# Optimization experiments

Hardware: AMD Instinct MI355X
Metric: run time of the kernel (lower is better)

## Reference

```python
import jax, jax.numpy as jnp
import numpy as np

D_MODEL = 512; FPQ = 15; SEQ = 2048; BSZ = 2
D_STATE = 16; D_CONV = 4; HEADDIM = 64; NHEADS = 16
D_INNER = 1024; CONV_DIM = D_INNER + 2 * D_STATE
D_IN_PROJ = 2 * D_INNER + 2 * D_STATE + NHEADS  # 2096
D_FF = 2048  # mlp_ratio 4.0 * 512
EPS_GATE = 0.01


def _rmsnorm(x, w, eps):
    xf = x.astype(jnp.float32)
    v = jnp.mean(xf * xf, axis=-1, keepdims=True)
    return w * (xf * jax.lax.rsqrt(v + eps)).astype(x.dtype)


def _mamba2(x, inproj, convw, convb, dtbias, Alog, Dp, normw, outproj):
    b, l, _ = x.shape
    zxbcdt = x @ inproj.T                      # [b,l,2096]
    z = zxbcdt[..., :D_INNER]
    xBC = zxbcdt[..., D_INNER:D_INNER + CONV_DIM]
    dt = zxbcdt[..., D_INNER + CONV_DIM:]      # [b,l,h]
    # causal depthwise conv1d (kernel D_CONV) + SiLU
    xp = jnp.pad(xBC, ((0, 0), (D_CONV - 1, 0), (0, 0)))
    conv = convb + sum(xp[:, k:k + l, :] * convw[:, k] for k in range(D_CONV))
    xBC = jax.nn.silu(conv)
    xs = xBC[..., :D_INNER]
    Bm = xBC[..., D_INNER:D_INNER + D_STATE]   # [b,l,n]
    Cm = xBC[..., D_INNER + D_STATE:]          # [b,l,n]
    dt = jax.nn.softplus(dt + dtbias)          # [b,l,h]
    A = -jnp.exp(Alog)                         # [h]
    xh = xs.reshape(b, l, NHEADS, HEADDIM)     # [b,l,h,p]
    dA = jnp.exp(dt * A)                       # [b,l,h]

    def step(hst, inp):
        dA_t, dt_t, B_t, x_t, C_t = inp        # [b,h],[b,h],[b,n],[b,h,p],[b,n]
        hst = dA_t[:, :, None, None] * hst + jnp.einsum('bh,bn,bhp->bhpn', dt_t, B_t, x_t)
        return hst, jnp.einsum('bhpn,bn->bhp', hst, C_t)

    h0 = jnp.zeros((b, NHEADS, HEADDIM, D_STATE), x.dtype)
    _, ys = jax.lax.scan(step, h0, (dA.transpose(1, 0, 2), dt.transpose(1, 0, 2),
                                    Bm.transpose(1, 0, 2), xh.transpose(1, 0, 2, 3),
                                    Cm.transpose(1, 0, 2)))
    y = ys.transpose(1, 0, 2, 3) + Dp[None, None, :, None] * xh  # [b,l,h,p]
    y = y.reshape(b, l, D_INNER) * jax.nn.silu(z)                # gated
    y = _rmsnorm(y, normw, 1e-5)
    return y @ outproj.T


def _forward(hidden_states, norm1_w, wfc_w, wfc_b, gfc_w, gfc_b,
             f_inproj, f_convw, f_convb, f_dtbias, f_Alog, f_D, f_normw, f_outproj,
             b_inproj, b_convw, b_convb, b_dtbias, b_Alog, b_D, b_normw, b_outproj,
             norm2_w, fc1_w, fc1_b, fc2_w, fc2_b):
    residual = hidden_states
    h = _rmsnorm(hidden_states, norm1_w, 1e-6)
    bsz, seq_len, d = h.shape
    cq = FPQ + 1
    nck = seq_len // cq
    h4 = h.reshape(bsz, nck, cq, d)
    frames = h4[:, :, :FPQ, :]                       # [b,nc,FPQ,d]
    queries = h4[:, :, FPQ, :]                       # [b,nc,d]
    alpha = jax.nn.softmax(queries @ wfc_w.T + wfc_b, axis=-1)   # [b,nc,FPQ]
    agg = jnp.einsum('bcfd,bcf->bcd', frames, alpha)
    gate = jax.nn.sigmoid(queries @ gfc_w.T + gfc_b)             # [b,nc,1]
    gate = gate * (1 - 2 * EPS_GATE) + EPS_GATE
    qn = queries * (1 - gate) + agg * gate
    h4 = jnp.concatenate([frames, qn[:, :, None, :]], axis=2)
    h = h4.reshape(bsz, seq_len, d)
    out_fwd = _mamba2(h, f_inproj, f_convw, f_convb, f_dtbias, f_Alog, f_D, f_normw, f_outproj)
    out_bwd = jnp.flip(_mamba2(jnp.flip(h, 1), b_inproj, b_convw, b_convb, b_dtbias, b_Alog, b_D, b_normw, b_outproj), 1)
    h = out_fwd + out_bwd + residual
    rm = h
    h = _rmsnorm(h, norm2_w, 1e-6)
    h = jax.nn.silu(h @ fc1_w.T + fc1_b) @ fc2_w.T + fc2_b
    h = h + rm
    return h + residual


def setup_inputs() -> dict:
    key = jax.random.key(0)
    ks = jax.random.split(key, 16)

    def n(k, shape, s=0.02):
        return s * jax.random.normal(k, shape, jnp.float32)

    def mixer(kb):
        k = jax.random.split(kb, 6)
        dtv = jnp.exp(jax.random.uniform(k[3], (NHEADS,), minval=jnp.log(1e-3), maxval=jnp.log(0.1)))
        return dict(
            inproj=n(k[0], (D_IN_PROJ, D_MODEL)),
            convw=n(k[1], (CONV_DIM, D_CONV), 0.2),
            convb=jnp.zeros((CONV_DIM,), jnp.float32),
            dtbias=jnp.log(jnp.expm1(dtv)),
            Alog=jnp.log(jax.random.uniform(k[4], (NHEADS,), minval=1.0, maxval=16.0)),
            D=jnp.ones((NHEADS,), jnp.float32),
            normw=jnp.ones((D_INNER,), jnp.float32),
            outproj=n(k[2], (D_MODEL, D_INNER)),
        )

    mf = mixer(ks[1]); mb = mixer(ks[2])
    inp = {
        'hidden_states': jax.random.normal(ks[0], (BSZ, SEQ, D_MODEL), jnp.float32),
        'norm1_w': jnp.ones((D_MODEL,), jnp.float32),
        'wfc_w': n(ks[3], (FPQ, D_MODEL)) * 0.001,
        'wfc_b': jnp.zeros((FPQ,), jnp.float32),
        'gfc_w': n(ks[4], (1, D_MODEL)) * 0.001,
        'gfc_b': jnp.zeros((1,), jnp.float32),
        'norm2_w': jnp.ones((D_MODEL,), jnp.float32),
        'fc1_w': n(ks[5], (D_FF, D_MODEL)),
        'fc1_b': jnp.zeros((D_FF,), jnp.float32),
        'fc2_w': n(ks[6], (D_MODEL, D_FF)),
        'fc2_b': jnp.zeros((D_MODEL,), jnp.float32),
    }
    for pre, m in (('f_', mf), ('b_', mb)):
        for kname, v in m.items():
            inp[pre + kname] = v
    return inp


def reference(hidden_states, norm1_w, wfc_w, wfc_b, gfc_w, gfc_b,
              f_inproj, f_convw, f_convb, f_dtbias, f_Alog, f_D, f_normw, f_outproj,
              b_inproj, b_convw, b_convb, b_dtbias, b_Alog, b_D, b_normw, b_outproj,
              norm2_w, fc1_w, fc1_b, fc2_w, fc2_b):
    return _forward(hidden_states, norm1_w, wfc_w, wfc_b, gfc_w, gfc_b,
                    f_inproj, f_convw, f_convb, f_dtbias, f_Alog, f_D, f_normw, f_outproj,
                    b_inproj, b_convw, b_convb, b_dtbias, b_Alog, b_D, b_normw, b_outproj,
                    norm2_w, fc1_w, fc1_b, fc2_w, fc2_b)
```

## Files before the change

kernel.cpp:

```cpp
#include <hip/hip_runtime.h>
#include <math.h>

#define SEQ 2048
#define BSZ 2
#define DM 512
#define DIN 1024
#define DSTATE 16
#define NH 16
#define HD 64
#define CONVDIM 1056
#define DINPROJ 2096
#define DFF 2048
#define ROWS (BSZ*SEQ)
#define NCH 32
#define CT  (SEQ/NCH)
#define ZXW 2176
#define ZXBN 8912896ull
#define BCN 65536ull
#define DTN 65536ull
#define YN  4194304ull
#define HSN 1048576ull

typedef short bf16x8 __attribute__((ext_vector_type(8)));
typedef float f32x4  __attribute__((ext_vector_type(4)));
typedef unsigned short u16x8 __attribute__((ext_vector_type(8)));

__device__ __forceinline__ float sigf(float x){ return 1.f/(1.f+expf(-x)); }

__device__ __forceinline__ unsigned short f2bf(float f){
  union { float f; unsigned u; } v; v.f = f;
  unsigned r = (v.u + 0x7FFFu + ((v.u >> 16) & 1u)) >> 16;
  return (unsigned short)r;
}
__device__ __forceinline__ float bf2f(unsigned short h){
  union { unsigned u; float f; } v; v.u = ((unsigned)h) << 16;
  return v.f;
}

template<int N> __device__ __forceinline__ void s_wait_vmcnt(){
  if constexpr (N == 0)      asm volatile("s_waitcnt vmcnt(0)" ::: "memory");
  else if constexpr (N == 1) asm volatile("s_waitcnt vmcnt(1)" ::: "memory");
  else if constexpr (N == 2) asm volatile("s_waitcnt vmcnt(2)" ::: "memory");
  else if constexpr (N == 3) asm volatile("s_waitcnt vmcnt(3)" ::: "memory");
  else if constexpr (N == 4) asm volatile("s_waitcnt vmcnt(4)" ::: "memory");
  else                       asm volatile("s_waitcnt vmcnt(8)" ::: "memory");
}

__device__ __forceinline__ float wave_reduce(float v){
#pragma unroll
  for (int o = 32; o > 0; o >>= 1) v += __shfl_down(v, o);
  return v;
}

__device__ __forceinline__ float block_reduce_256(float v, float* sbuf){
  v = wave_reduce(v);
  int lane = threadIdx.x & 63, wid = threadIdx.x >> 6;
  if (lane == 0) sbuf[wid] = v;
  __syncthreads();
  float s = sbuf[0] + sbuf[1] + sbuf[2] + sbuf[3];
  __syncthreads();
  return s;
}

__global__ __launch_bounds__(256)
void castpad2_k(const float* __restrict__ in0, const float* __restrict__ in1,
                unsigned short* __restrict__ out0, unsigned short* __restrict__ out1,
                int N, int K, int Npad){
  int tot = Npad*K;
  int idx = blockIdx.x*256 + threadIdx.x;
  const float* in = in0; unsigned short* out = out0;
  if (idx >= tot){ idx -= tot; in = in1; out = out1; }
  if (idx >= tot) return;
  int n = idx / K, k = idx - n*K;
  out[idx] = (n < N) ? f2bf(in[(size_t)n*K + k]) : (unsigned short)0;
}

struct Cast6 {
  const float* src[6];
  unsigned short* dst[6];
  int n[6];
};
__global__ __launch_bounds__(256)
void cast6_k(Cast6 cp){
  int seg = blockIdx.y;
  int n4 = cp.n[seg] >> 2;
  int i = blockIdx.x*256 + threadIdx.x;
  if (i >= n4) return;
  const float* src = cp.src[seg];
  unsigned short* dst = cp.dst[seg];
  float4 v = *(const float4*)&src[i*4];
  ushort4 o;
  o.x = f2bf(v.x); o.y = f2bf(v.y); o.z = f2bf(v.z); o.w = f2bf(v.w);
  *(ushort4*)&dst[i*4] = o;
}

__global__ __launch_bounds__(256)
void rmsnorm512_k(const float* __restrict__ x, const float* __restrict__ w,
                  float* __restrict__ y, unsigned short* __restrict__ yb, float eps){
  __shared__ float sbuf[4];
  int r = blockIdx.x;
  const float* xr = x + (size_t)r*DM;
  float v0 = xr[threadIdx.x];
  float v1 = xr[threadIdx.x + 256];
  float ss = block_reduce_256(v0*v0 + v1*v1, sbuf);
  float rs = rsqrtf(ss*(1.f/DM) + eps);
  float o0 = w[threadIdx.x]*v0*rs;
  float o1 = w[threadIdx.x+256]*v1*rs;
  y[(size_t)r*DM + threadIdx.x]       = o0;
  y[(size_t)r*DM + threadIdx.x + 256] = o1;
  yb[(size_t)r*DM + threadIdx.x]       = f2bf(o0);
  yb[(size_t)r*DM + threadIdx.x + 256] = f2bf(o1);
}

__global__ __launch_bounds__(256)
void gated_fusion_k(float* __restrict__ h, unsigned short* __restrict__ hb,
                    const float* __restrict__ wfc_w, const float* __restrict__ wfc_b,
                    const float* __restrict__ gfc_w, const float* __restrict__ gfc_b){
  int c = blockIdx.x;
  float* base = h + (size_t)c*16*DM;
  float* qrow = base + 15*DM;
  unsigned short* qrow_b = hb + (size_t)c*16*DM + 15*DM;
  __shared__ float q[DM];
  __shared__ float dots[16];
  for (int i = threadIdx.x; i < DM; i += 256) q[i] = qrow[i];
  __syncthreads();
  int wid = threadIdx.x >> 6, lane = threadIdx.x & 63;
  for (int f = wid; f < 16; f += 4){
    const float* wf = (f < 15) ? (wfc_w + (size_t)f*DM) : gfc_w;
    float s = 0.f;
    for (int i = lane; i < DM; i += 64) s += q[i]*wf[i];
    s = wave_reduce(s);
    if (lane == 0) dots[f] = s;
  }
  __syncthreads();
  if (threadIdx.x == 0){
    float mx = -1e30f;
    for (int f = 0; f < 15; f++){ dots[f] += wfc_b[f]; mx = fmaxf(mx, dots[f]); }
    float sum = 0.f;
    for (int f = 0; f < 15; f++){ float e = expf(dots[f]-mx); dots[f] = e; sum += e; }
    float inv = 1.f/sum;
    for (int f = 0; f < 15; f++) dots[f] *= inv;
    float g = sigf(dots[15] + gfc_b[0]);
    dots[15] = g*0.98f + 0.01f;
  }
  __syncthreads();
  float gate = dots[15];
  for (int d = threadIdx.x; d < DM; d += 256){
    float agg = 0.f;
#pragma unroll
    for (int f = 0; f < 15; f++) agg += base[(size_t)f*DM + d]*dots[f];
    float qn = q[d]*(1.f-gate) + agg*gate;
    qrow[d] = qn;
    qrow_b[d] = f2bf(qn);
  }
}

template<int NW, int WM, int WN, int FM, int FN, int DEPTH, int NBUF>
__global__ __launch_bounds__(NW*64)
void mgemm_k(const unsigned short* __restrict__ A, size_t Astride,
             const unsigned short* __restrict__ W0, const unsigned short* __restrict__ W1,
             const float* __restrict__ bias, const float* __restrict__ add1,
             const float* __restrict__ add2, float* __restrict__ Cf,
             unsigned short* __restrict__ Cb, size_t Cstride,
             int K, int Nreal, int flipArg, int act){
  constexpr int BM = WM*FM*16;
  constexpr int BN = WN*FN*16;
  constexpr int NG = (BM+BN)/16;
  constexpr int L  = NG/NW;
  static_assert(NG % NW == 0, "staging must be uniform per wave");
  constexpr int BUFS = (BM+BN)*32;
  __shared__ __align__(16) unsigned short S[NBUF*BUFS];
  int tid = threadIdx.x;
  int w = tid >> 6, lane = tid & 63;
  int gx = gridDim.x;
  int nwg = gx*gridDim.y;
  int bid = blockIdx.x + gx*blockIdx.y;
  int swz = (bid & 7)*(nwg >> 3) + (bid >> 3);
  int n0 = (swz % gx)*BN, m0 = (swz / gx)*BM;
  int dir = blockIdx.z;
  const unsigned short* Aa = A + (size_t)dir*Astride;
  const unsigned short* Wd = dir ? W1 : W0;
  int flip = (flipArg < 0) ? dir : flipArg;
  int wr = w / WN, wc = w % WN;

  f32x4 acc[FM][FN];
#pragma unroll
  for (int i = 0; i < FM; i++)
#pragma unroll
    for (int j = 0; j < FN; j++)
#pragma unroll
      for (int r = 0; r < 4; r++) acc[i][j][r] = 0.f;

  const unsigned short* gp[L];
  int gdst[L];
#pragma unroll
  for (int gi = 0; gi < L; gi++){
    int g = w + gi*NW;
    int r16 = lane >> 2, cch = lane & 3;
    int r = g*16 + r16;
    const unsigned short* src;
    if (r < BM){
      int gm = m0 + r;
      if (flip) gm = (gm & ~(SEQ-1)) | ((SEQ-1) - (gm & (SEQ-1)));
      src = Aa + (size_t)gm*K;
    } else {
      src = Wd + (size_t)(n0 + (r - BM))*K;
    }
    int c2 = (cch + ((r16 >> 1) & 3)) & 3;
    gp[gi] = src + c2*8;
    gdst[gi] = g*16*32;
  }
  int aoff[FM], boff[FN];
#pragma unroll
  for (int i = 0; i < FM; i++){
    int R = wr*FM*16 + i*16 + (lane & 15);
    int slot = ((lane >> 4) - ((R >> 1) & 3)) & 3;
    aoff[i] = R*32 + slot*8;
  }
#pragma unroll
  for (int j = 0; j < FN; j++){
    int R = BM + wc*FN*16 + j*16 + (lane & 15);
    int slot = ((lane >> 4) - ((R >> 1) & 3)) & 3;
    boff[j] = R*32 + slot*8;
  }

  int T = K >> 5;
#pragma unroll
  for (int jt = 0; jt < DEPTH; jt++){
#pragma unroll
    for (int gi = 0; gi < L; gi++)
      __builtin_amdgcn_global_load_lds(
        (const __attribute__((address_space(1))) void*)(gp[gi] + (jt << 5)),
        (__attribute__((address_space(3))) void*)&S[jt*BUFS + gdst[gi]], 16, 0, 0);
  }

  int cs = 0;
  for (int t = 0; t < T; t++){
    int rem = T - 1 - t;
    if (rem >= DEPTH-1)             s_wait_vmcnt<L*(DEPTH-1)>();
    else if constexpr (DEPTH >= 3){ if (rem == 1) s_wait_vmcnt<L>(); else s_wait_vmcnt<0>(); }
    else                            s_wait_vmcnt<0>();
    __builtin_amdgcn_s_barrier();
    __builtin_amdgcn_sched_barrier(0);
    const unsigned short* buf = &S[cs*BUFS];
    bf16x8 af[FM], bfr[FN];
#pragma unroll
    for (int i = 0; i < FM; i++) af[i] = *(const bf16x8*)&buf[aoff[i]];
#pragma unroll
    for (int j = 0; j < FN; j++) bfr[j] = *(const bf16x8*)&buf[boff[j]];
    if constexpr (NBUF == DEPTH){
      asm volatile("s_waitcnt lgkmcnt(0)" ::: "memory");
      __builtin_amdgcn_sched_barrier(0);
      __builtin_amdgcn_s_barrier();
    }
    if (t + DEPTH < T){
      int ss = cs + DEPTH; if (ss >= NBUF) ss -= NBUF;
#pragma unroll
      for (int gi = 0; gi < L; gi++)
        __builtin_amdgcn_global_load_lds(
          (const __attribute__((address_space(1))) void*)(gp[gi] + ((t + DEPTH) << 5)),
          (__attribute__((address_space(3))) void*)&S[ss*BUFS + gdst[gi]], 16, 0, 0);
    }
#pragma unroll
    for (int i = 0; i < FM; i++)
#pragma unroll
      for (int j = 0; j < FN; j++)
        acc[i][j] = __builtin_amdgcn_mfma_f32_16x16x32_bf16(af[i], bfr[j], acc[i][j], 0, 0, 0);
    cs = (cs + 1 == NBUF) ? 0 : cs + 1;
  }

  float* Cfd = Cf ? Cf + (size_t)dir*Cstride : nullptr;
  unsigned short* Cbd = Cb ? Cb + (size_t)dir*Cstride : nullptr;

  if (Cbd){
    __syncthreads();
#pragma unroll
    for (int i = 0; i < FM; i++){
#pragma unroll
      for (int j = 0; j < FN; j++){
        int col = wc*FN*16 + j*16 + (lane & 15);
        float bv = bias ? bias[n0 + col] : 0.f;
#pragma unroll
        for (int r = 0; r < 4; r++){
          int row = wr*FM*16 + i*16 + (lane >> 4)*4 + r;
          float x = acc[i][j][r] + bv;
          if (act) x = x*sigf(x);
          S[row*BN + (col ^ ((row & 3) << 3))] = f2bf(x);
        }
      }
    }
    __syncthreads();
    constexpr int TOT8 = BM*BN/8;
    for (int s = tid; s < TOT8; s += NW*64){
      int idx = s*8;
      int row = idx / BN, col = idx % BN;
      u16x8 v = *(const u16x8*)&S[row*BN + (col ^ ((row & 3) << 3))];
      *(u16x8*)&Cbd[(size_t)(m0 + row)*Nreal + n0 + col] = v;
    }
    return;
  }

  int mbase = m0 + wr*FM*16 + (lane >> 4)*4;
  int nbase = n0 + wc*FN*16 + (lane & 15);
#pragma unroll
  for (int i = 0; i < FM; i++){
#pragma unroll
    for (int j = 0; j < FN; j++){
      int col = nbase + j*16;
      if (col < Nreal){
        float bv = bias ? bias[col] : 0.f;
#pragma unroll
        for (int r = 0; r < 4; r++){
          size_t idx = (size_t)(mbase + i*16 + r)*Nreal + col;
          float x = acc[i][j][r] + bv;
          if (act) x = x*sigf(x);
          if (add1) x += add1[idx] + add2[idx];
          Cfd[idx] = x;
        }
      }
    }
  }
}

__global__ __launch_bounds__(128)
void convbc_dt_k(const unsigned short* __restrict__ zxb,
                 const float* __restrict__ convw0, const float* __restrict__ convw1,
                 const float* __restrict__ convb0, const float* __restrict__ convb1,
                 const float* __restrict__ dtbias0, const float* __restrict__ dtbias1,
                 const float* __restrict__ Alog0, const float* __restrict__ Alog1,
                 float* __restrict__ Bm, float* __restrict__ Cm,
                 float* __restrict__ dtv, float* __restrict__ dAv){
  int dir = blockIdx.y;
  const unsigned short* zb = zxb + (size_t)dir*ZXBN;
  int r0 = blockIdx.x*4;
  int l0 = r0 & (SEQ-1);
  int rbase = r0 - l0;
  int tid = threadIdx.x;
  if (tid < 32){
    const float* convw = dir ? convw1 : convw0;
    const float* convb = dir ? convb1 : convb0;
    int cc = 1024 + tid;
    int col = 2048 + tid;
    float w0 = convw[cc*4+0], w1 = convw[cc*4+1], w2 = convw[cc*4+2], w3 = convw[cc*4+3];
    float bv = convb[cc];
    float v[7];
#pragma unroll
    for (int i = 0; i < 7; i++){
      int ls = l0 - 3 + i;
      v[i] = (ls >= 0) ? bf2f(zb[(size_t)(rbase+ls)*ZXW + col]) : 0.f;
    }
#pragma unroll
    for (int j = 0; j < 4; j++){
      float acc = bv + v[j]*w0 + v[j+1]*w1 + v[j+2]*w2 + v[j+3]*w3;
      float val = acc*sigf(acc);
      int r = r0 + j;
      if (tid < 16) Bm[(size_t)dir*BCN + (size_t)r*DSTATE + tid] = val;
      else          Cm[(size_t)dir*BCN + (size_t)r*DSTATE + (tid-16)] = val;
    }
  } else if (tid >= 64){
    const float* dtbias = dir ? dtbias1 : dtbias0;
    const float* Alog   = dir ? Alog1 : Alog0;
    int i = tid - 64;
    int j = i >> 4, hh = i & 15;
    int r = r0 + j;
    float x = bf2f(zb[(size_t)r*ZXW + 2080 + hh]) + dtbias[hh];
    float sp = (x > 20.f) ? x : log1pf(expf(x));
    dtv[(size_t)dir*DTN + (size_t)r*NH + hh] = sp;
    dAv[(size_t)dir*DTN + (size_t)r*NH + hh] = expf(-expf(Alog[hh])*sp);
  }
}

__global__ __launch_bounds__(64)
void scanA_k(const unsigned short* __restrict__ zxb, const float* __restrict__ Bm,
             const float* __restrict__ Cm, const float* __restrict__ dtv,
             const float* __restrict__ dAv,
             const float* __restrict__ convw0, const float* __restrict__ convw1,
             const float* __restrict__ convb0, const float* __restrict__ convb1,
             const float* __restrict__ Dp0, const float* __restrict__ Dp1,
             unsigned short* __restrict__ y,
             float* __restrict__ Hs, float* __restrict__ Ps){
  int gb = blockIdx.x;
  int dir = gb >> 10;
  int idx = gb & 1023;
  int c = idx & (NCH-1);
  int h = (idx >> 5) & 15;
  int b = idx >> 9;
  int p = threadIdx.x;
  int t0 = c*CT;
  __shared__ __align__(16) float sB[CT][16];
  __shared__ __align__(16) float sC[CT][16];
  __shared__ float sdt[CT];
  __shared__ float sdA[CT];
  const unsigned short* zb = zxb + (size_t)dir*ZXBN;
  const unsigned short* zcol = zb + ((size_t)b*SEQ)*ZXW + 1024 + h*HD + p;
  unsigned short* yb = y + (size_t)dir*YN + ((size_t)b*SEQ + t0)*DIN + h*HD;
  const float* Bb  = Bm + (size_t)dir*BCN + ((size_t)b*SEQ + t0)*DSTATE;
  const float* Cb  = Cm + (size_t)dir*BCN + ((size_t)b*SEQ + t0)*DSTATE;
  const float* dtb = dtv + (size_t)dir*DTN + ((size_t)b*SEQ + t0)*NH + h;
  const float* dAb = dAv + (size_t)dir*DTN + ((size_t)b*SEQ + t0)*NH + h;
  const float* convw = dir ? convw1 : convw0;
  const float* convb = dir ? convb1 : convb0;
  float Dv = (dir ? Dp1 : Dp0)[h];
  int ch = h*HD + p;
  float cw0 = convw[ch*4+0], cw1 = convw[ch*4+1], cw2 = convw[ch*4+2], cw3 = convw[ch*4+3];
  float cbv = convb[ch];
#pragma unroll
  for (int k = 0; k < (CT*16)/64; k++){
    int i = p + k*64;
    ((float*)sB)[i] = Bb[i];
    ((float*)sC)[i] = Cb[i];
  }
  sdt[p] = dtb[(size_t)p*NH];
  sdA[p] = dAb[(size_t)p*NH];
  __syncthreads();

  float hst[16];
#pragma unroll
  for (int n = 0; n < 16; n++) hst[n] = 0.f;
  float P = 1.f;
  float carry0 = (t0 >= 3) ? bf2f(zcol[(size_t)(t0-3)*ZXW]) : 0.f;
  float carry1 = (t0 >= 2) ? bf2f(zcol[(size_t)(t0-2)*ZXW]) : 0.f;
  float carry2 = (t0 >= 1) ? bf2f(zcol[(size_t)(t0-1)*ZXW]) : 0.f;
  float cur[16], nxt[16];
#pragma unroll
  for (int j = 0; j < 16; j++) cur[j] = bf2f(zcol[(size_t)(t0+j)*ZXW]);

  for (int tt = 0; tt < CT; tt += 16){
    bool pf = (tt + 16 < CT);
    if (pf){
#pragma unroll
      for (int j = 0; j < 16; j++) nxt[j] = bf2f(zcol[(size_t)(t0+tt+16+j)*ZXW]);
    }
    float win[19];
    win[0] = carry0; win[1] = carry1; win[2] = carry2;
#pragma unroll
    for (int j = 0; j < 16; j++) win[3+j] = cur[j];
#pragma unroll
    for (int j = 0; j < 16; j++){
      int t = tt + j;
      float xo = cbv + win[j]*cw0 + win[j+1]*cw1 + win[j+2]*cw2 + win[j+3]*cw3;
      float xsil = xo*sigf(xo);
      float xv = xsil*sdt[t];
      float dA = sdA[t];
      P *= dA;
      float4 b0 = *(const float4*)&sB[t][0];
      float4 b1 = *(const float4*)&sB[t][4];
      float4 b2 = *(const float4*)&sB[t][8];
      float4 b3 = *(const float4*)&sB[t][12];
      hst[0]  = fmaf(dA, hst[0],  b0.x*xv);
      hst[1]  = fmaf(dA, hst[1],  b0.y*xv);
      hst[2]  = fmaf(dA, hst[2],  b0.z*xv);
      hst[3]  = fmaf(dA, hst[3],  b0.w*xv);
      hst[4]  = fmaf(dA, hst[4],  b1.x*xv);
      hst[5]  = fmaf(dA, hst[5],  b1.y*xv);
      hst[6]  = fmaf(dA, hst[6],  b1.z*xv);
      hst[7]  = fmaf(dA, hst[7],  b1.w*xv);
      hst[8]  = fmaf(dA, hst[8],  b2.x*xv);
      hst[9]  = fmaf(dA, hst[9],  b2.y*xv);
      hst[10] = fmaf(dA, hst[10], b2.z*xv);
      hst[11] = fmaf(dA, hst[11], b2.w*xv);
      hst[12] = fmaf(dA, hst[12], b3.x*xv);
      hst[13] = fmaf(dA, hst[13], b3.y*xv);
      hst[14] = fmaf(dA, hst[14], b3.z*xv);
      hst[15] = fmaf(dA, hst[15], b3.w*xv);
      float4 c0 = *(const float4*)&sC[t][0];
      float4 c1 = *(const float4*)&sC[t][4];
      float4 c2 = *(const float4*)&sC[t][8];
      float4 c3 = *(const float4*)&sC[t][12];
      float a0 = hst[0]*c0.x;  a0 = fmaf(hst[1],  c0.y, a0);
      a0 = fmaf(hst[2],  c0.z, a0); a0 = fmaf(hst[3],  c0.w, a0);
      float a1 = hst[4]*c1.x;  a1 = fmaf(hst[5],  c1.y, a1);
      a1 = fmaf(hst[6],  c1.z, a1); a1 = fmaf(hst[7],  c1.w, a1);
      float a2 = hst[8]*c2.x;  a2 = fmaf(hst[9],  c2.y, a2);
      a2 = fmaf(hst[10], c2.z, a2); a2 = fmaf(hst[11], c2.w, a2);
      float a3 = hst[12]*c3.x; a3 = fmaf(hst[13], c3.y, a3);
      a3 = fmaf(hst[14], c3.z, a3); a3 = fmaf(hst[15], c3.w, a3);
      float dot = (a0+a1)+(a2+a3);
      yb[(size_t)t*DIN + p] = f2bf(dot + Dv*xsil);
    }
    carry0 = cur[13]; carry1 = cur[14]; carry2 = cur[15];
    if (pf){
#pragma unroll
      for (int j = 0; j < 16; j++) cur[j] = nxt[j];
    }
  }
  size_t base = (size_t)dir*HSN + ((size_t)((b*NH + h)*NCH + c))*1024;
#pragma unroll
  for (int n = 0; n < 16; n++) Hs[base + n*64 + p] = hst[n];
  if (p == 0) Ps[dir*1024 + (b*NH + h)*NCH + c] = P;
}

__global__ __launch_bounds__(64)
void scanC_k(const float* __restrict__ Cm, const float* __restrict__ dAv,
             const float* __restrict__ Hs, const float* __restrict__ Ps,
             unsigned short* __restrict__ y){
  int gb = blockIdx.x;
  int dir = gb >> 10;
  int idx = gb & 1023;
  int c = idx & (NCH-1);
  if (c == 0) return;
  int h = (idx >> 5) & 15;
  int b = idx >> 9;
  int p = threadIdx.x;
  int t0 = c*CT;
  int bh = b*NH + h;
  float hstart[16];
#pragma unroll
  for (int n = 0; n < 16; n++) hstart[n] = 0.f;
  for (int j = 0; j < c; j++){
    float Pj = Ps[dir*1024 + bh*NCH + j];
    const float* Hj = Hs + (size_t)dir*HSN + ((size_t)(bh*NCH + j))*1024;
#pragma unroll
    for (int n = 0; n < 16; n++) hstart[n] = fmaf(Pj, hstart[n], Hj[n*64 + p]);
  }
  __shared__ __align__(16) float sC[CT][16];
  __shared__ float sdA[CT];
  const float* Cb  = Cm + (size_t)dir*BCN + ((size_t)b*SEQ + t0)*DSTATE;
  const float* dAb = dAv + (size_t)dir*DTN + ((size_t)b*SEQ + t0)*NH + h;
  unsigned short* yb = y + (size_t)dir*YN + ((size_t)b*SEQ + t0)*DIN + h*HD;
#pragma unroll
  for (int k = 0; k < (CT*16)/64; k++){
    int i = p + k*64;
    ((float*)sC)[i] = Cb[i];
  }
  sdA[p] = dAb[(size_t)p*NH];
  __syncthreads();

  float cp = 1.f;
  float ycur[16], ynxt[16];
#pragma unroll
  for (int j = 0; j < 16; j++) ycur[j] = bf2f(yb[(size_t)j*DIN + p]);
  for (int tt = 0; tt < CT; tt += 16){
    bool pf = (tt + 16 < CT);
    if (pf){
#pragma unroll
      for (int j = 0; j < 16; j++) ynxt[j] = bf2f(yb[(size_t)(tt+16+j)*DIN + p]);
    }
#pragma unroll
    for (int j = 0; j < 16; j++){
      int t = tt + j;
      cp *= sdA[t];
      float4 c0 = *(const float4*)&sC[t][0];
      float4 c1 = *(const float4*)&sC[t][4];
      float4 c2 = *(const float4*)&sC[t][8];
      float4 c3 = *(const float4*)&sC[t][12];
      float a0 = hstart[0]*c0.x;  a0 = fmaf(hstart[1],  c0.y, a0);
      a0 = fmaf(hstart[2],  c0.z, a0); a0 = fmaf(hstart[3],  c0.w, a0);
      float a1 = hstart[4]*c1.x;  a1 = fmaf(hstart[5],  c1.y, a1);
      a1 = fmaf(hstart[6],  c1.z, a1); a1 = fmaf(hstart[7],  c1.w, a1);
      float a2 = hstart[8]*c2.x;  a2 = fmaf(hstart[9],  c2.y, a2);
      a2 = fmaf(hstart[10], c2.z, a2); a2 = fmaf(hstart[11], c2.w, a2);
      float a3 = hstart[12]*c3.x; a3 = fmaf(hstart[13], c3.y, a3);
      a3 = fmaf(hstart[14], c3.z, a3); a3 = fmaf(hstart[15], c3.w, a3);
      float dot = (a0+a1)+(a2+a3);
      yb[(size_t)t*DIN + p] = f2bf(ycur[j] + cp*dot);
    }
    if (pf){
#pragma unroll
      for (int j = 0; j < 16; j++) ycur[j] = ynxt[j];
    }
  }
}

__global__ __launch_bounds__(256)
void gated_rms_k(const unsigned short* __restrict__ y,
                 const unsigned short* __restrict__ zxb,
                 const float* __restrict__ nw0, const float* __restrict__ nw1,
                 unsigned short* __restrict__ out){
  __shared__ float sbuf[4];
  int r = blockIdx.x;
  int dir = blockIdx.y;
  const float* normw = dir ? nw1 : nw0;
  const unsigned short* yr = y + (size_t)dir*YN + (size_t)r*DIN;
  const unsigned short* zr = zxb + (size_t)dir*ZXBN + (size_t)r*ZXW;
  unsigned short* outr = out + (size_t)dir*((size_t)ROWS*DIN) + (size_t)r*DIN;
  int d0 = threadIdx.x*4;
  ushort4 yu4 = *(const ushort4*)&yr[d0];
  ushort4 zu4 = *(const ushort4*)&zr[d0];
  float vals[4]; float ss = 0.f;
  float yv[4] = {bf2f(yu4.x), bf2f(yu4.y), bf2f(yu4.z), bf2f(yu4.w)};
  float zv[4] = {bf2f(zu4.x), bf2f(zu4.y), bf2f(zu4.z), bf2f(zu4.w)};
#pragma unroll
  for (int i = 0; i < 4; i++){
    float g = yv[i] * (zv[i]*sigf(zv[i]));
    vals[i] = g; ss += g*g;
  }
  ss = block_reduce_256(ss, sbuf);
  float rs = rsqrtf(ss*(1.f/DIN) + 1e-5f);
  ushort4 o;
  o.x = f2bf(normw[d0+0]*vals[0]*rs);
  o.y = f2bf(normw[d0+1]*vals[1]*rs);
  o.z = f2bf(normw[d0+2]*vals[2]*rs);
  o.w = f2bf(normw[d0+3]*vals[3]*rs);
  *(ushort4*)&outr[d0] = o;
}

__global__ __launch_bounds__(256)
void addres_rms_k(const float* __restrict__ outf, const float* __restrict__ outb,
                  const float* __restrict__ hid, const float* __restrict__ w,
                  float* __restrict__ hsum, unsigned short* __restrict__ h2b){
  __shared__ float sbuf[4];
  int r = blockIdx.x;
  int l = r & (SEQ-1);
  int rb = (r - l) + ((SEQ-1) - l);
  float vals[2]; float ss = 0.f;
#pragma unroll
  for (int i = 0; i < 2; i++){
    int d = threadIdx.x + i*256;
    float v = outf[(size_t)r*DM + d] + outb[(size_t)rb*DM + d] + hid[(size_t)r*DM + d];
    hsum[(size_t)r*DM + d] = v;
    vals[i] = v; ss += v*v;
  }
  ss = block_reduce_256(ss, sbuf);
  float rs = rsqrtf(ss*(1.f/DM) + 1e-6f);
#pragma unroll
  for (int i = 0; i < 2; i++){
    int d = threadIdx.x + i*256;
    h2b[(size_t)r*DM + d] = f2bf(w[d]*vals[i]*rs);
  }
}

extern "C" void kernel_launch(void* const* d_in, const int* in_sizes, int n_in,
                              void* d_out, int out_size, void* d_ws, size_t ws_size,
                              hipStream_t stream){
  const float* hid     = (const float*)d_in[0];
  const float* norm1_w = (const float*)d_in[1];
  const float* wfc_w   = (const float*)d_in[2];
  const float* wfc_b   = (const float*)d_in[3];
  const float* gfc_w   = (const float*)d_in[4];
  const float* gfc_b   = (const float*)d_in[5];
  const float* norm2_w = (const float*)d_in[6];
  const float* fc1_w   = (const float*)d_in[7];
  const float* fc1_b   = (const float*)d_in[8];
  const float* fc2_w   = (const float*)d_in[9];
  const float* fc2_b   = (const float*)d_in[10];
  const float* inproj[2]  = {(const float*)d_in[11], (const float*)d_in[19]};
  const float* convw[2]   = {(const float*)d_in[12], (const float*)d_in[20]};
  const float* convb[2]   = {(const float*)d_in[13], (const float*)d_in[21]};
  const float* dtbias[2]  = {(const float*)d_in[14], (const float*)d_in[22]};
  const float* Alog[2]    = {(const float*)d_in[15], (const float*)d_in[23]};
  const float* Dp[2]      = {(const float*)d_in[16], (const float*)d_in[24]};
  const float* normw[2]   = {(const float*)d_in[17], (const float*)d_in[25]};
  const float* outproj[2] = {(const float*)d_in[18], (const float*)d_in[26]};

  float* ws = (float*)d_ws;
  unsigned short* zxb = (unsigned short*)ws;
  float* Bmb   = ws + 8912896;
  float* Cmb   = Bmb + 2*BCN;
  float* dtv   = Cmb + 2*BCN;
  float* dAv   = dtv + 2*DTN;
  float* ysc   = dAv + 2*DTN;
  unsigned short* ysc_b = (unsigned short*)ysc;
  float* Ps    = ysc + 4194304;
  float* outd  = Ps + 2048;
  float* hsum  = outd + 4194304;
  float* hnorm = hsum + 2097152;
  unsigned short* hnorm_bf = (unsigned short*)(hnorm + 2097152);
  unsigned short* ysc_bf   = (unsigned short*)(hnorm + 2097152 + 1048576);
  unsigned short* wbf      = (unsigned short*)(hnorm + 2097152 + 1048576 + 4194304);
  float* Hs = hsum;
  unsigned short* a1_bf = (unsigned short*)zxb;
  unsigned short* h2_bf = (unsigned short*)ysc;
  unsigned short* wi0 = wbf,            * wi1 = wbf + 1114112;
  unsigned short* wo0 = wbf + 2228224,  * wo1 = wbf + 2752512;
  unsigned short* wf1 = wbf + 3276800;
  unsigned short* wf2 = wbf + 4325376;
  size_t need_bytes = (size_t)29952000*4;
  if (ws_size < need_bytes) return;

  castpad2_k<<<(2*2176*512)/256, 256, 0, stream>>>(inproj[0], inproj[1], wi0, wi1, 2096, 512, 2176);
  Cast6 cp;
  cp.src[0] = outproj[0]; cp.dst[0] = wo0; cp.n[0] = 512*1024;
  cp.src[1] = outproj[1]; cp.dst[1] = wo1; cp.n[1] = 512*1024;
  cp.src[2] = fc1_w; cp.dst[2] = wf1; cp.n[2] = 2048*512;
  cp.src[3] = fc2_w; cp.dst[3] = wf2; cp.n[3] = 512*2048;
  cp.src[4] = fc2_w; cp.dst[4] = wf2; cp.n[4] = 0;
  cp.src[5] = fc2_w; cp.dst[5] = wf2; cp.n[5] = 0;
  cast6_k<<<dim3((2048*512/4)/256, 4), 256, 0, stream>>>(cp);

  rmsnorm512_k<<<ROWS, 256, 0, stream>>>(hid, norm1_w, hnorm, hnorm_bf, 1e-6f);
  gated_fusion_k<<<BSZ*(SEQ/16), 256, 0, stream>>>(hnorm, hnorm_bf, wfc_w, wfc_b, gfc_w, gfc_b);

  mgemm_k<8,2,4,4,2,2,2><<<dim3(2176/128, 4096/128, 2), 512, 0, stream>>>(
      hnorm_bf, 0, wi0, wi1, nullptr, nullptr, nullptr, nullptr, zxb, ZXBN,
      512, ZXW, -1, 0);
  convbc_dt_k<<<dim3(ROWS/4, 2), 128, 0, stream>>>(
      zxb, convw[0], convw[1], convb[0], convb[1], dtbias[0], dtbias[1],
      Alog[0], Alog[1], Bmb, Cmb, dtv, dAv);
  scanA_k<<<2*BSZ*NH*NCH, 64, 0, stream>>>(
      zxb, Bmb, Cmb, dtv, dAv, convw[0], convw[1], convb[0], convb[1],
      Dp[0], Dp[1], ysc_b, Hs, Ps);
  scanC_k<<<2*BSZ*NH*NCH, 64, 0, stream>>>(Cmb, dAv, Hs, Ps, ysc_b);
  gated_rms_k<<<dim3(ROWS, 2), 256, 0, stream>>>(
      ysc_b, zxb, normw[0], normw[1], ysc_bf);
  mgemm_k<8,2,4,2,1,3,4><<<dim3(512/64, 4096/64, 2), 512, 0, stream>>>(
      ysc_bf, (size_t)ROWS*DIN, wo0, wo1, nullptr, nullptr, nullptr,
      outd, nullptr, 2097152, 1024, DM, 0, 0);

  addres_rms_k<<<ROWS, 256, 0, stream>>>(outd, outd + 2097152, hid, norm2_w, hsum, h2_bf);
  mgemm_k<8,2,4,4,2,3,3><<<dim3(2048/128, 4096/128, 1), 512, 0, stream>>>(
      h2_bf, 0, wf1, wf1, fc1_b, nullptr, nullptr, nullptr, a1_bf, 0,
      512, DFF, 0, 1);
  mgemm_k<8,2,4,2,1,3,4><<<dim3(512/64, 4096/64, 1), 512, 0, stream>>>(
      a1_bf, 0, wf2, wf2, fc2_b, hsum, hid, (float*)d_out, nullptr, 0,
      2048, DM, 0, 0);
}
```

Before: 195.3 us.

## Double scan chunk count and add a separate sequential chunk-state prefix kernel

Doubles the number of chunks in the chunked selective scan (32 to 64) so each scanA/scanC block handles 32 timesteps, doubling the parallel blocks. The quadratic per-block prefix over previous chunk states in scanC is replaced by a new scanB kernel that computes every chunk's starting state once with one sequential pass per (dir,batch,head). This adds a kernel launch and a small serial pass of 64 blocks, plus extra workspace traffic for the Hstart buffer, in exchange for less redundant work and more parallelism.

```diff
diff --git a/kernel.cpp b/kernel.cpp
--- a/kernel.cpp
+++ b/kernel.cpp
@@ -12,14 +12,14 @@
 #define DINPROJ 2096
 #define DFF 2048
 #define ROWS (BSZ*SEQ)
-#define NCH 32
+#define NCH 64
 #define CT  (SEQ/NCH)
 #define ZXW 2176
 #define ZXBN 8912896ull
 #define BCN 65536ull
 #define DTN 65536ull
 #define YN  4194304ull
-#define HSN 1048576ull
+#define HSN 2097152ull
 
 typedef short bf16x8 __attribute__((ext_vector_type(8)));
 typedef float f32x4  __attribute__((ext_vector_type(4)));
@@ -380,11 +380,11 @@
              unsigned short* __restrict__ y,
              float* __restrict__ Hs, float* __restrict__ Ps){
   int gb = blockIdx.x;
-  int dir = gb >> 10;
-  int idx = gb & 1023;
+  int dir = gb >> 11;
+  int idx = gb & 2047;
   int c = idx & (NCH-1);
-  int h = (idx >> 5) & 15;
-  int b = idx >> 9;
+  int h = (idx >> 6) & 15;
+  int b = idx >> 10;
   int p = threadIdx.x;
   int t0 = c*CT;
   __shared__ __align__(16) float sB[CT][16];
@@ -410,8 +410,10 @@
     ((float*)sB)[i] = Bb[i];
     ((float*)sC)[i] = Cb[i];
   }
-  sdt[p] = dtb[(size_t)p*NH];
-  sdA[p] = dAb[(size_t)p*NH];
+  if (p < CT){
+    sdt[p] = dtb[(size_t)p*NH];
+    sdA[p] = dAb[(size_t)p*NH];
+  }
   __syncthreads();
 
   float hst[16];
@@ -487,32 +489,51 @@
   size_t base = (size_t)dir*HSN + ((size_t)((b*NH + h)*NCH + c))*1024;
 #pragma unroll
   for (int n = 0; n < 16; n++) Hs[base + n*64 + p] = hst[n];
-  if (p == 0) Ps[dir*1024 + (b*NH + h)*NCH + c] = P;
+  if (p == 0) Ps[dir*2048 + (b*NH + h)*NCH + c] = P;
+}
+
+__global__ __launch_bounds__(64)
+void scanB_k(const float* __restrict__ Hs, const float* __restrict__ Ps,
+             float* __restrict__ Hstart){
+  int g = blockIdx.x;
+  int dir = g >> 5;
+  int bh = g & 31;
+  int p = threadIdx.x;
+  size_t base = (size_t)dir*HSN + (size_t)bh*NCH*1024;
+  const float* Pp = Ps + dir*2048 + bh*NCH;
+  float s[16];
+#pragma unroll
+  for (int n = 0; n < 16; n++) s[n] = 0.f;
+#pragma unroll 2
+  for (int c = 1; c < NCH; c++){
+    float Pj = Pp[c-1];
+    const float* Hj = Hs + base + (size_t)(c-1)*1024;
+#pragma unroll
+    for (int n = 0; n < 16; n++) s[n] = fmaf(Pj, s[n], Hj[n*64 + p]);
+    float* Oc = Hstart + base + (size_t)c*1024;
+#pragma unroll
+    for (int n = 0; n < 16; n++) Oc[n*64 + p] = s[n];
+  }
 }
 
 __global__ __launch_bounds__(64)
 void scanC_k(const float* __restrict__ Cm, const float* __restrict__ dAv,
-             const float* __restrict__ Hs, const float* __restrict__ Ps,
+             const float* __restrict__ Hstart,
              unsigned short* __restrict__ y){
   int gb = blockIdx.x;
-  int dir = gb >> 10;
-  int idx = gb & 1023;
+  int dir = gb >> 11;
+  int idx = gb & 2047;
   int c = idx & (NCH-1);
   if (c == 0) return;
-  int h = (idx >> 5) & 15;
-  int b = idx >> 9;
+  int h = (idx >> 6) & 15;
+  int b = idx >> 10;
   int p = threadIdx.x;
   int t0 = c*CT;
   int bh = b*NH + h;
   float hstart[16];
-#pragma unroll
-  for (int n = 0; n < 16; n++) hstart[n] = 0.f;
-  for (int j = 0; j < c; j++){
-    float Pj = Ps[dir*1024 + bh*NCH + j];
-    const float* Hj = Hs + (size_t)dir*HSN + ((size_t)(bh*NCH + j))*1024;
-#pragma unroll
-    for (int n = 0; n < 16; n++) hstart[n] = fmaf(Pj, hstart[n], Hj[n*64 + p]);
-  }
+  const float* Hj = Hstart + (size_t)dir*HSN + ((size_t)(bh*NCH + c))*1024;
+#pragma unroll
+  for (int n = 0; n < 16; n++) hstart[n] = Hj[n*64 + p];
   __shared__ __align__(16) float sC[CT][16];
   __shared__ float sdA[CT];
   const float* Cb  = Cm + (size_t)dir*BCN + ((size_t)b*SEQ + t0)*DSTATE;
@@ -523,7 +544,7 @@
     int i = p + k*64;
     ((float*)sC)[i] = Cb[i];
   }
-  sdA[p] = dAb[(size_t)p*NH];
+  if (p < CT) sdA[p] = dAb[(size_t)p*NH];
   __syncthreads();
 
   float cp = 1.f;
@@ -652,20 +673,21 @@
   float* ysc   = dAv + 2*DTN;
   unsigned short* ysc_b = (unsigned short*)ysc;
   float* Ps    = ysc + 4194304;
-  float* outd  = Ps + 2048;
+  float* outd  = Ps + 4096;
   float* hsum  = outd + 4194304;
   float* hnorm = hsum + 2097152;
   unsigned short* hnorm_bf = (unsigned short*)(hnorm + 2097152);
   unsigned short* ysc_bf   = (unsigned short*)(hnorm + 2097152 + 1048576);
   unsigned short* wbf      = (unsigned short*)(hnorm + 2097152 + 1048576 + 4194304);
-  float* Hs = hsum;
+  float* Hs = outd;
+  float* Hstart = hsum;
   unsigned short* a1_bf = (unsigned short*)zxb;
   unsigned short* h2_bf = (unsigned short*)ysc;
   unsigned short* wi0 = wbf,            * wi1 = wbf + 1114112;
   unsigned short* wo0 = wbf + 2228224,  * wo1 = wbf + 2752512;
   unsigned short* wf1 = wbf + 3276800;
   unsigned short* wf2 = wbf + 4325376;
-  size_t need_bytes = (size_t)29952000*4;
+  size_t need_bytes = (size_t)29954048*4;
   if (ws_size < need_bytes) return;
 
   castpad2_k<<<(2*2176*512)/256, 256, 0, stream>>>(inproj[0], inproj[1], wi0, wi1, 2096, 512, 2176);
@@ -690,7 +712,8 @@
   scanA_k<<<2*BSZ*NH*NCH, 64, 0, stream>>>(
       zxb, Bmb, Cmb, dtv, dAv, convw[0], convw[1], convb[0], convb[1],
       Dp[0], Dp[1], ysc_b, Hs, Ps);
-  scanC_k<<<2*BSZ*NH*NCH, 64, 0, stream>>>(Cmb, dAv, Hs, Ps, ysc_b);
+  scanB_k<<<64, 64, 0, stream>>>(Hs, Ps, Hstart);
+  scanC_k<<<2*BSZ*NH*NCH, 64, 0, stream>>>(Cmb, dAv, Hstart, ysc_b);
   gated_rms_k<<<dim3(ROWS, 2), 256, 0, stream>>>(
       ysc_b, zxb, normw[0], normw[1], ysc_bf);
   mgemm_k<8,2,4,2,1,3,4><<<dim3(512/64, 4096/64, 2), 512, 0, stream>>>(
```

Result: slower. 202.6 us (+3.8%).
